# Optimization experiments

Measured on AMD Instinct MI355X. Metric: run time of the kernel, lower is better.

The kernel has to match this reference:

```python
import jax, jax.numpy as jnp
import numpy as np
import math

NUM_HEADS = 8  # init kwarg num_heads


def setup_inputs() -> dict:
    key = jax.random.key(0)
    k1, k2, k3, k4, k5 = jax.random.split(key, 5)
    n, q, kv, d, W = 2048, 256, 256, 64, 64  # n = batch(4) * windows(64) * heads(8)
    return {
        "queries": jax.random.normal(k1, (n, q, d), jnp.float32),
        "keys": jax.random.normal(k2, (n, kv, d), jnp.float32),
        "values": jax.random.normal(k3, (n, kv, d), jnp.float32),
        "valid_lens": jax.random.randint(k5, (n,), 0, 256, jnp.int32),
        "window_mask": jax.random.normal(k4, (W, q, kv), jnp.float32),
    }


def reference(queries, keys, values, valid_lens, window_mask):
    d = queries.shape[-1]
    # scores = Q K^T / sqrt(d)
    scores = jnp.einsum('bqd,bkd->bqk', queries, keys) / math.sqrt(d)
    n, q, kv = scores.shape
    W = window_mask.shape[0]
    # additive Swin-style window mask, broadcast over batch and heads
    scores = (scores.reshape(n // (W * NUM_HEADS), W, NUM_HEADS, q, kv)
              + window_mask[None, :, None]).reshape(n, q, kv)
    # masked softmax: multiply valid entries, add -1e6 to invalid (matches _sequence_mask)
    mask = (jnp.arange(kv)[None, None, :] < valid_lens[:, None, None]).astype(scores.dtype)
    scores = scores * mask + (1.0 - mask) * (-1e6)
    attn = jax.nn.softmax(scores, axis=-1)
    # dropout p=0.0 -> identity
    return jnp.einsum('bqk,bkd->bqd', attn, values)
```

## Files before the change

### kernel.cpp

```cpp
#include <hip/hip_runtime.h>
#include <stdint.h>

typedef __attribute__((ext_vector_type(8))) short short8;
typedef __attribute__((ext_vector_type(4))) float floatx4;

#define SEQQ 256
#define SEQK 256
#define HD   64
#define KSTR 72
#define VTSTR 264
#define PSTR 40

__device__ __forceinline__ unsigned short f2b(float x) {
    union { float f; uint32_t u; } v; v.f = x;
    return (unsigned short)((v.u + 0x7FFFu + ((v.u >> 16) & 1u)) >> 16);
}
__device__ __forceinline__ uint32_t pack2(float a, float b) {
    return (uint32_t)f2b(a) | ((uint32_t)f2b(b) << 16);
}

__global__ __launch_bounds__(256) void attn_fused(
    const float* __restrict__ Qg, const float* __restrict__ Kg,
    const float* __restrict__ Vg, const int* __restrict__ Lg,
    const float* __restrict__ WMg, float* __restrict__ Og)
{
    __shared__ __align__(16) unsigned short ldsKV[SEQK * KSTR];
    __shared__ __align__(16) unsigned short ldsP[4 * 2 * 16 * PSTR];

    const int tid   = threadIdx.x;
    const int lane  = tid & 63;
    const int wave  = tid >> 6;
    const int row16 = lane & 15;
    const int quad  = lane >> 4;

    const int bidx  = blockIdx.x;
    const int batch = bidx >> 2;
    const int qb    = bidx & 3;
    const int q0    = qb * 64 + wave * 16;

    const float* qptr = Qg + (size_t)batch * SEQQ * HD;
    const float* kptr = Kg + (size_t)batch * SEQK * HD;
    const float* vptr = Vg + (size_t)batch * SEQK * HD;
    const float* wptr = WMg + (size_t)((batch >> 3) & 63) * SEQQ * SEQK;
    const int L = Lg[batch];

    #pragma unroll
    for (int it = 0; it < 32; ++it) {
        int pe  = it * 256 + tid;
        int kvr = pe >> 5;
        int pi  = pe & 31;
        const float2 f = *(const float2*)(kptr + kvr * HD + pi * 2);
        *(uint32_t*)&ldsKV[kvr * KSTR + pi * 2] = pack2(f.x, f.y);
    }

    short8 qf0, qf1;
    {
        const float* qr = qptr + (q0 + row16) * HD + quad * 8;
        float4 a = *(const float4*)(qr);
        float4 b = *(const float4*)(qr + 4);
        float4 c = *(const float4*)(qr + 32);
        float4 d = *(const float4*)(qr + 36);
        qf0 = (short8){ (short)f2b(a.x),(short)f2b(a.y),(short)f2b(a.z),(short)f2b(a.w),
                        (short)f2b(b.x),(short)f2b(b.y),(short)f2b(b.z),(short)f2b(b.w) };
        qf1 = (short8){ (short)f2b(c.x),(short)f2b(c.y),(short)f2b(c.z),(short)f2b(c.w),
                        (short)f2b(d.x),(short)f2b(d.y),(short)f2b(d.z),(short)f2b(d.w) };
    }

    __syncthreads();

    floatx4 acc[16];
    #pragma unroll
    for (int j = 0; j < 16; ++j) acc[j] = (floatx4){0.f, 0.f, 0.f, 0.f};
    #pragma unroll
    for (int j = 0; j < 16; ++j) {
        const unsigned short* kb = &ldsKV[(j * 16 + row16) * KSTR + quad * 8];
        short8 kf0 = *(const short8*)kb;
        short8 kf1 = *(const short8*)(kb + 32);
        acc[j] = __builtin_amdgcn_mfma_f32_16x16x32_bf16(qf0, kf0, acc[j], 0, 0, 0);
        acc[j] = __builtin_amdgcn_mfma_f32_16x16x32_bf16(qf1, kf1, acc[j], 0, 0, 0);
    }

    float inv[4];
    #pragma unroll
    for (int r = 0; r < 4; ++r) {
        const int qrow = q0 + quad * 4 + r;
        const float* wr = wptr + qrow * SEQK + row16;
        float mx = -3.0e38f;
        #pragma unroll
        for (int j = 0; j < 16; ++j) {
            float s = acc[j][r] * 0.125f + wr[16 * j];
            s = (16 * j + row16 < L) ? s : -1.0e6f;
            acc[j][r] = s;
            mx = fmaxf(mx, s);
        }
        #pragma unroll
        for (int o = 1; o < 16; o <<= 1) mx = fmaxf(mx, __shfl_xor(mx, o, 64));
        float sm = 0.f;
        #pragma unroll
        for (int j = 0; j < 16; ++j) {
            float e = exp2f((acc[j][r] - mx) * 1.44269504088896f);
            acc[j][r] = e;
            sm += e;
        }
        #pragma unroll
        for (int o = 1; o < 16; o <<= 1) sm += __shfl_xor(sm, o, 64);
        inv[r] = __builtin_amdgcn_rcpf(sm);
    }

    __syncthreads();

    #pragma unroll 4
    for (int it = 0; it < 16; ++it) {
        int p4 = it * 256 + tid;
        int d  = p4 & 63;
        int k4 = p4 >> 6;
        int kv = k4 * 4;
        float v0 = vptr[(kv + 0) * HD + d];
        float v1 = vptr[(kv + 1) * HD + d];
        float v2 = vptr[(kv + 2) * HD + d];
        float v3 = vptr[(kv + 3) * HD + d];
        uint2 pk; pk.x = pack2(v0, v1); pk.y = pack2(v2, v3);
        *(uint2*)&ldsKV[d * VTSTR + kv] = pk;
    }

    __syncthreads();

    floatx4 oacc[4];
    #pragma unroll
    for (int t = 0; t < 4; ++t) oacc[t] = (floatx4){0.f, 0.f, 0.f, 0.f};
    unsigned short* psbase = &ldsP[wave * 2 * 16 * PSTR];
    #pragma unroll
    for (int c = 0; c < 8; ++c) {
        unsigned short* ps = psbase + (c & 1) * 16 * PSTR;
        #pragma unroll
        for (int r = 0; r < 4; ++r) {
            const int prow = quad * 4 + r;
            ps[prow * PSTR + row16]      = f2b(acc[2 * c    ][r] * inv[r]);
            ps[prow * PSTR + 16 + row16] = f2b(acc[2 * c + 1][r] * inv[r]);
        }
        __asm__ __volatile__("" ::: "memory");
        __builtin_amdgcn_s_waitcnt(0xC07F);
        short8 pf = *(const short8*)&ps[row16 * PSTR + quad * 8];
        #pragma unroll
        for (int t = 0; t < 4; ++t) {
            short8 vf = *(const short8*)&ldsKV[(t * 16 + row16) * VTSTR + c * 32 + quad * 8];
            oacc[t] = __builtin_amdgcn_mfma_f32_16x16x32_bf16(pf, vf, oacc[t], 0, 0, 0);
        }
    }

    float* op = Og + (size_t)batch * SEQQ * HD;
    #pragma unroll
    for (int t = 0; t < 4; ++t) {
        #pragma unroll
        for (int r = 0; r < 4; ++r) {
            op[(q0 + quad * 4 + r) * HD + t * 16 + row16] = oacc[t][r];
        }
    }
}

extern "C" void kernel_launch(void* const* d_in, const int* in_sizes, int n_in,
                              void* d_out, int out_size, void* d_ws, size_t ws_size,
                              hipStream_t stream) {
    const float* Qg = (const float*)d_in[0];
    const float* Kg = (const float*)d_in[1];
    const float* Vg = (const float*)d_in[2];
    const int*   Lg = (const int*)d_in[3];
    const float* Wm = (const float*)d_in[4];
    float* Og = (float*)d_out;

    const int nbatch = in_sizes[3];
    dim3 grid(nbatch * 4), block(256);
    hipLaunchKernelGGL(attn_fused, grid, block, 0, stream, Qg, Kg, Vg, Lg, Wm, Og);
}
```

Measured before the change: 509.7 us.

## Pre-convert window mask to bf16, widen K loads, overlap V staging with softmax

```diff
diff --git a/kernel.cpp b/kernel.cpp
--- a/kernel.cpp
+++ b/kernel.cpp
@@ -11,18 +11,34 @@
 #define VTSTR 264
 #define PSTR 40
 
+__device__ __forceinline__ uint32_t rpack2(float a, float b) {
+    uint32_t ua = __builtin_bit_cast(uint32_t, a) + 0x8000u;
+    uint32_t ub = __builtin_bit_cast(uint32_t, b) + 0x8000u;
+    return __builtin_amdgcn_perm(ub, ua, 0x07060302u);
+}
 __device__ __forceinline__ unsigned short f2b(float x) {
-    union { float f; uint32_t u; } v; v.f = x;
-    return (unsigned short)((v.u + 0x7FFFu + ((v.u >> 16) & 1u)) >> 16);
-}
-__device__ __forceinline__ uint32_t pack2(float a, float b) {
-    return (uint32_t)f2b(a) | ((uint32_t)f2b(b) << 16);
-}
-
+    return (unsigned short)((__builtin_bit_cast(uint32_t, x) + 0x8000u) >> 16);
+}
+__device__ __forceinline__ float b2f(unsigned short b) {
+    return __builtin_bit_cast(float, ((uint32_t)b) << 16);
+}
+
+__global__ __launch_bounds__(256) void wm_convert(const float* __restrict__ wm,
+                                                  unsigned short* __restrict__ out) {
+    int i = (blockIdx.x * 256 + threadIdx.x) * 8;
+    float4 a = *(const float4*)(wm + i);
+    float4 b = *(const float4*)(wm + i + 4);
+    uint4 o;
+    o.x = rpack2(a.x, a.y); o.y = rpack2(a.z, a.w);
+    o.z = rpack2(b.x, b.y); o.w = rpack2(b.z, b.w);
+    *(uint4*)(out + i) = o;
+}
+
+template <bool WMBF16>
 __global__ __launch_bounds__(256) void attn_fused(
     const float* __restrict__ Qg, const float* __restrict__ Kg,
     const float* __restrict__ Vg, const int* __restrict__ Lg,
-    const float* __restrict__ WMg, float* __restrict__ Og)
+    const void* __restrict__ WMg, float* __restrict__ Og)
 {
     __shared__ __align__(16) unsigned short ldsKV[SEQK * KSTR];
     __shared__ __align__(16) unsigned short ldsP[4 * 2 * 16 * PSTR];
@@ -41,16 +57,17 @@
     const float* qptr = Qg + (size_t)batch * SEQQ * HD;
     const float* kptr = Kg + (size_t)batch * SEQK * HD;
     const float* vptr = Vg + (size_t)batch * SEQK * HD;
-    const float* wptr = WMg + (size_t)((batch >> 3) & 63) * SEQQ * SEQK;
+    const size_t wmoff = (size_t)((batch >> 3) & 63) * SEQQ * SEQK;
     const int L = Lg[batch];
 
     #pragma unroll
-    for (int it = 0; it < 32; ++it) {
+    for (int it = 0; it < 16; ++it) {
         int pe  = it * 256 + tid;
-        int kvr = pe >> 5;
-        int pi  = pe & 31;
-        const float2 f = *(const float2*)(kptr + kvr * HD + pi * 2);
-        *(uint32_t*)&ldsKV[kvr * KSTR + pi * 2] = pack2(f.x, f.y);
+        int kvr = pe >> 4;
+        int pi  = pe & 15;
+        const float4 f = *(const float4*)(kptr + kvr * HD + pi * 4);
+        uint2 pk; pk.x = rpack2(f.x, f.y); pk.y = rpack2(f.z, f.w);
+        *(uint2*)&ldsKV[kvr * KSTR + pi * 4] = pk;
     }
 
     short8 qf0, qf1;
@@ -60,10 +77,12 @@
         float4 b = *(const float4*)(qr + 4);
         float4 c = *(const float4*)(qr + 32);
         float4 d = *(const float4*)(qr + 36);
-        qf0 = (short8){ (short)f2b(a.x),(short)f2b(a.y),(short)f2b(a.z),(short)f2b(a.w),
-                        (short)f2b(b.x),(short)f2b(b.y),(short)f2b(b.z),(short)f2b(b.w) };
-        qf1 = (short8){ (short)f2b(c.x),(short)f2b(c.y),(short)f2b(c.z),(short)f2b(c.w),
-                        (short)f2b(d.x),(short)f2b(d.y),(short)f2b(d.z),(short)f2b(d.w) };
+        union { short8 s; uint32_t u[4]; } t0, t1;
+        t0.u[0] = rpack2(a.x, a.y); t0.u[1] = rpack2(a.z, a.w);
+        t0.u[2] = rpack2(b.x, b.y); t0.u[3] = rpack2(b.z, b.w);
+        t1.u[0] = rpack2(c.x, c.y); t1.u[1] = rpack2(c.z, c.w);
+        t1.u[2] = rpack2(d.x, d.y); t1.u[3] = rpack2(d.z, d.w);
+        qf0 = t0.s; qf1 = t1.s;
     }
 
     __syncthreads();
@@ -80,15 +99,39 @@
         acc[j] = __builtin_amdgcn_mfma_f32_16x16x32_bf16(qf1, kf1, acc[j], 0, 0, 0);
     }
 
+    __syncthreads();
+
+    #pragma unroll 4
+    for (int it = 0; it < 16; ++it) {
+        int p4 = it * 256 + tid;
+        int d  = p4 & 63;
+        int kv = (p4 >> 6) * 4;
+        float v0 = vptr[(kv + 0) * HD + d];
+        float v1 = vptr[(kv + 1) * HD + d];
+        float v2 = vptr[(kv + 2) * HD + d];
+        float v3 = vptr[(kv + 3) * HD + d];
+        uint2 pk; pk.x = rpack2(v0, v1); pk.y = rpack2(v2, v3);
+        *(uint2*)&ldsKV[d * VTSTR + kv] = pk;
+    }
+
     float inv[4];
     #pragma unroll
     for (int r = 0; r < 4; ++r) {
         const int qrow = q0 + quad * 4 + r;
-        const float* wr = wptr + qrow * SEQK + row16;
+        float wv[16];
+        if (WMBF16) {
+            const unsigned short* wr = (const unsigned short*)WMg + wmoff + qrow * SEQK + row16;
+            #pragma unroll
+            for (int j = 0; j < 16; ++j) wv[j] = b2f(wr[16 * j]);
+        } else {
+            const float* wr = (const float*)WMg + wmoff + qrow * SEQK + row16;
+            #pragma unroll
+            for (int j = 0; j < 16; ++j) wv[j] = wr[16 * j];
+        }
         float mx = -3.0e38f;
         #pragma unroll
         for (int j = 0; j < 16; ++j) {
-            float s = acc[j][r] * 0.125f + wr[16 * j];
+            float s = acc[j][r] * 0.125f + wv[j];
             s = (16 * j + row16 < L) ? s : -1.0e6f;
             acc[j][r] = s;
             mx = fmaxf(mx, s);
@@ -105,22 +148,6 @@
         #pragma unroll
         for (int o = 1; o < 16; o <<= 1) sm += __shfl_xor(sm, o, 64);
         inv[r] = __builtin_amdgcn_rcpf(sm);
-    }
-
-    __syncthreads();
-
-    #pragma unroll 4
-    for (int it = 0; it < 16; ++it) {
-        int p4 = it * 256 + tid;
-        int d  = p4 & 63;
-        int k4 = p4 >> 6;
-        int kv = k4 * 4;
-        float v0 = vptr[(kv + 0) * HD + d];
-        float v1 = vptr[(kv + 1) * HD + d];
-        float v2 = vptr[(kv + 2) * HD + d];
-        float v3 = vptr[(kv + 3) * HD + d];
-        uint2 pk; pk.x = pack2(v0, v1); pk.y = pack2(v2, v3);
-        *(uint2*)&ldsKV[d * VTSTR + kv] = pk;
     }
 
     __syncthreads();
@@ -169,6 +196,16 @@
     float* Og = (float*)d_out;
 
     const int nbatch = in_sizes[3];
-    dim3 grid(nbatch * 4), block(256);
-    hipLaunchKernelGGL(attn_fused, grid, block, 0, stream, Qg, Kg, Vg, Lg, Wm, Og);
-}
+    const int wm_elems = in_sizes[4];
+    dim3 block(256);
+
+    if ((size_t)wm_elems * sizeof(unsigned short) <= ws_size) {
+        unsigned short* wmb = (unsigned short*)d_ws;
+        hipLaunchKernelGGL(wm_convert, dim3(wm_elems / 2048), block, 0, stream, Wm, wmb);
+        hipLaunchKernelGGL((attn_fused<true>), dim3(nbatch * 4), block, 0, stream,
+                           Qg, Kg, Vg, Lg, (const void*)wmb, Og);
+    } else {
+        hipLaunchKernelGGL((attn_fused<false>), dim3(nbatch * 4), block, 0, stream,
+                           Qg, Kg, Vg, Lg, (const void*)Wm, Og);
+    }
+}
```

Result: faster. 472.6 us (-7.3%).
